# Optimization experiments

Hardware: AMD Instinct MI355X
Metric: run time of the kernel (lower is better)

The kernel has to match this reference:

```python
import jax, jax.numpy as jnp
import numpy as np
from jax import lax

N_GAUSS = 4096


def setup_inputs() -> dict:
    key = jax.random.key(0)
    k1, k2, k3, k4 = jax.random.split(key, 4)
    return {
        "_xyz": jax.random.normal(k1, (N_GAUSS, 3), dtype=jnp.float32),
        "_scaling": jax.random.normal(k2, (N_GAUSS, 3), dtype=jnp.float32),
        "_rotation": jax.random.normal(k3, (N_GAUSS, 4), dtype=jnp.float32),
        "_opacity": jax.random.normal(k4, (N_GAUSS, 1), dtype=jnp.float32),
        "resolution": 64,
        "num_blocks": 16,
    }


def _extract_fields(_xyz, _scaling, _rotation, _opacity, resolution, num_blocks):
    relax_ratio = 1.5
    block_size = 2.0 / num_blocks
    split_size = resolution // num_blocks

    # opacity activation + threshold mask (kept dense; masked gaussians get 0 weight)
    opacities = jax.nn.sigmoid(_opacity)[:, 0]  # [N]
    keep = opacities > 0.005
    opa = jnp.where(keep, opacities, 0.0)

    BIG = jnp.float32(1e10)
    mn = jnp.min(jnp.where(keep[:, None], _xyz, BIG), axis=0)
    mx = jnp.max(jnp.where(keep[:, None], _xyz, -BIG), axis=0)
    center = (mn + mx) / 2
    scale = 1.8 / jnp.max(mx - mn)
    xyzs = (_xyz - center) * scale           # [N,3] normalized positions
    stds = jnp.exp(_scaling) * scale         # [N,3] scaling activation * scale

    # covariance from scaling+rotation: L = R @ diag(s); C = L L^T
    q = _rotation / jnp.linalg.norm(_rotation, axis=1, keepdims=True)
    r, x, y, z = q[:, 0], q[:, 1], q[:, 2], q[:, 3]
    R = jnp.stack([
        jnp.stack([1 - 2 * (y * y + z * z), 2 * (x * y - r * z), 2 * (x * z + r * y)], -1),
        jnp.stack([2 * (x * y + r * z), 1 - 2 * (x * x + z * z), 2 * (y * z - r * x)], -1),
        jnp.stack([2 * (x * z - r * y), 2 * (y * z + r * x), 1 - 2 * (x * x + y * y)], -1),
    ], axis=1)                               # [N,3,3]
    L = R * stds[:, None, :]                 # R @ diag(s)
    C = jnp.einsum('nij,nkj->nik', L, L)     # [N,3,3]
    a, b, c = C[:, 0, 0], C[:, 0, 1], C[:, 0, 2]
    d, e, f = C[:, 1, 1], C[:, 1, 2], C[:, 2, 2]

    # analytic 3x3 symmetric inverse (precomputed per gaussian)
    inv_det = 1.0 / (a * d * f + 2 * e * c * b - e * e * a - c * c * d - b * b * f + 1e-24)
    inv_a = (d * f - e * e) * inv_det
    inv_b = (e * c - b * f) * inv_det
    inv_c = (e * b - c * d) * inv_det
    inv_d = (a * f - c * c) * inv_det
    inv_e = (b * c - e * a) * inv_det
    inv_f = (a * d - b * b) * inv_det

    lin = jnp.linspace(-1.0, 1.0, resolution).astype(jnp.float32)
    nb = num_blocks
    bi, bj, bk = jnp.meshgrid(jnp.arange(nb), jnp.arange(nb), jnp.arange(nb), indexing='ij')
    blocks = jnp.stack([bi.ravel(), bj.ravel(), bk.ravel()], axis=1)  # [nb^3, 3]
    off = jnp.arange(split_size)
    relax = block_size * relax_ratio

    def block_val(blk):
        xs = lin[blk[0] * split_size + off]
        ys = lin[blk[1] * split_size + off]
        zs = lin[blk[2] * split_size + off]
        xx, yy, zz = jnp.meshgrid(xs, ys, zs, indexing='ij')
        pts = jnp.stack([xx.ravel(), yy.ravel(), zz.ravel()], axis=-1)  # [S^3, 3]
        vmin = pts.min(0) - relax
        vmax = pts.max(0) + relax
        inside = jnp.all((xyzs < vmax) & (xyzs > vmin), axis=1)  # [N]
        w_opa = jnp.where(inside, opa, 0.0)                      # [N]
        dxyz = pts[:, None, :] - xyzs[None, :, :]                # [S^3, N, 3]
        px, py, pz = dxyz[..., 0], dxyz[..., 1], dxyz[..., 2]
        power = (-0.5 * (px * px * inv_a + py * py * inv_d + pz * pz * inv_f)
                 - px * py * inv_b - px * pz * inv_c - py * pz * inv_e)
        power = jnp.where(power > 0, jnp.float32(-1e10), power)
        val = jnp.sum(w_opa * jnp.exp(power), axis=1)            # [S^3]
        return val.reshape(split_size, split_size, split_size)

    vals = lax.map(block_val, blocks)  # [nb^3, S, S, S]
    occ = (vals.reshape(nb, nb, nb, split_size, split_size, split_size)
               .transpose(0, 3, 1, 4, 2, 5)
               .reshape(resolution, resolution, resolution))
    return occ


def reference(_xyz, _scaling, _rotation, _opacity, resolution, num_blocks):
    return _extract_fields(_xyz, _scaling, _rotation, _opacity, resolution, num_blocks)
```

## Files before the change

kernel.cpp:

```cpp
#include <hip/hip_runtime.h>

#define NG 4096
#define RELAX 0.1875f
#define KEEPTH -5.2933049f
#define SLICES 8
#define SLICE_G (NG/SLICES)
#define EV_THREADS 256

__device__ __forceinline__ float linf(int i) { return -1.0f + (2.0f/63.0f)*(float)i; }

__global__ __launch_bounds__(256) void gm_prep(
    const float* __restrict__ xyz, const float* __restrict__ scal,
    const float* __restrict__ rot, const float* __restrict__ opac,
    float4* __restrict__ posopa, float4* __restrict__ invrec,
    float4* __restrict__ out4)
{
  __shared__ float s_r[4][6];
  const int tid = threadIdx.x;
  const int b   = blockIdx.x;
  const float4* xyz4 = (const float4*)xyz;
  const float4* op4  = (const float4*)opac;

  {
    const int t0 = b*256 + tid;
    #pragma unroll
    for (int i = 0; i < 16; ++i) out4[t0 + i*4096] = make_float4(0,0,0,0);
  }

  float mn0=1e10f, mn1=1e10f, mn2=1e10f;
  float mx0=-1e10f, mx1=-1e10f, mx2=-1e10f;
  #pragma unroll
  for (int t = 0; t < 4; ++t) {
    const int G = t*256 + tid;
    float4 v0 = xyz4[3*G+0], v1 = xyz4[3*G+1], v2 = xyz4[3*G+2];
    float4 oo = op4[G];
    if (oo.x > KEEPTH) { mn0=fminf(mn0,v0.x); mx0=fmaxf(mx0,v0.x);
                         mn1=fminf(mn1,v0.y); mx1=fmaxf(mx1,v0.y);
                         mn2=fminf(mn2,v0.z); mx2=fmaxf(mx2,v0.z); }
    if (oo.y > KEEPTH) { mn0=fminf(mn0,v0.w); mx0=fmaxf(mx0,v0.w);
                         mn1=fminf(mn1,v1.x); mx1=fmaxf(mx1,v1.x);
                         mn2=fminf(mn2,v1.y); mx2=fmaxf(mx2,v1.y); }
    if (oo.z > KEEPTH) { mn0=fminf(mn0,v1.z); mx0=fmaxf(mx0,v1.z);
                         mn1=fminf(mn1,v1.w); mx1=fmaxf(mx1,v1.w);
                         mn2=fminf(mn2,v2.x); mx2=fmaxf(mx2,v2.x); }
    if (oo.w > KEEPTH) { mn0=fminf(mn0,v2.y); mx0=fmaxf(mx0,v2.y);
                         mn1=fminf(mn1,v2.z); mx1=fmaxf(mx1,v2.z);
                         mn2=fminf(mn2,v2.w); mx2=fmaxf(mx2,v2.w); }
  }
  #pragma unroll
  for (int s = 1; s < 64; s <<= 1) {
    mn0 = fminf(mn0, __shfl_xor(mn0, s)); mx0 = fmaxf(mx0, __shfl_xor(mx0, s));
    mn1 = fminf(mn1, __shfl_xor(mn1, s)); mx1 = fmaxf(mx1, __shfl_xor(mx1, s));
    mn2 = fminf(mn2, __shfl_xor(mn2, s)); mx2 = fmaxf(mx2, __shfl_xor(mx2, s));
  }
  if ((tid & 63) == 0) {
    const int w = tid >> 6;
    s_r[w][0]=mn0; s_r[w][1]=mn1; s_r[w][2]=mn2;
    s_r[w][3]=mx0; s_r[w][4]=mx1; s_r[w][5]=mx2;
  }
  __syncthreads();
  mn0 = fminf(fminf(s_r[0][0],s_r[1][0]), fminf(s_r[2][0],s_r[3][0]));
  mn1 = fminf(fminf(s_r[0][1],s_r[1][1]), fminf(s_r[2][1],s_r[3][1]));
  mn2 = fminf(fminf(s_r[0][2],s_r[1][2]), fminf(s_r[2][2],s_r[3][2]));
  mx0 = fmaxf(fmaxf(s_r[0][3],s_r[1][3]), fmaxf(s_r[2][3],s_r[3][3]));
  mx1 = fmaxf(fmaxf(s_r[0][4],s_r[1][4]), fmaxf(s_r[2][4],s_r[3][4]));
  mx2 = fmaxf(fmaxf(s_r[0][5],s_r[1][5]), fmaxf(s_r[2][5],s_r[3][5]));
  const float cx = (mn0+mx0)*0.5f;
  const float cy = (mn1+mx1)*0.5f;
  const float cz = (mn2+mx2)*0.5f;
  const float sc = 1.8f/fmaxf(mx0-mn0, fmaxf(mx1-mn1, mx2-mn2));

  const int g = b*256 + tid;
  float o = opac[g];
  float sig = 1.0f/(1.0f + __expf(-o));
  float opa = (sig > 0.005f) ? sig : 0.0f;
  float xs = (xyz[3*g+0]-cx)*sc;
  float ys = (xyz[3*g+1]-cy)*sc;
  float zs = (xyz[3*g+2]-cz)*sc;
  float sdx = __expf(scal[3*g+0])*sc;
  float sdy = __expf(scal[3*g+1])*sc;
  float sdz = __expf(scal[3*g+2])*sc;
  float qr=rot[4*g+0], qx=rot[4*g+1], qy=rot[4*g+2], qz=rot[4*g+3];
  float qn = 1.0f/sqrtf(qr*qr+qx*qx+qy*qy+qz*qz);
  qr*=qn; qx*=qn; qy*=qn; qz*=qn;
  float R00 = 1.0f-2.0f*(qy*qy+qz*qz), R01 = 2.0f*(qx*qy-qr*qz), R02 = 2.0f*(qx*qz+qr*qy);
  float R10 = 2.0f*(qx*qy+qr*qz), R11 = 1.0f-2.0f*(qx*qx+qz*qz), R12 = 2.0f*(qy*qz-qr*qx);
  float R20 = 2.0f*(qx*qz-qr*qy), R21 = 2.0f*(qy*qz+qr*qx), R22 = 1.0f-2.0f*(qx*qx+qy*qy);
  float L00=R00*sdx, L01=R01*sdy, L02=R02*sdz;
  float L10=R10*sdx, L11=R11*sdy, L12=R12*sdz;
  float L20=R20*sdx, L21=R21*sdy, L22=R22*sdz;
  float a = L00*L00+L01*L01+L02*L02;
  float bb= L00*L10+L01*L11+L02*L12;
  float cc= L00*L20+L01*L21+L02*L22;
  float d = L10*L10+L11*L11+L12*L12;
  float e = L10*L20+L11*L21+L12*L22;
  float f = L20*L20+L21*L21+L22*L22;
  float det = a*d*f + 2.0f*e*cc*bb - e*e*a - cc*cc*d - bb*bb*f + 1e-24f;
  float idt = 1.0f/det;
  float ia=(d*f-e*e)*idt, ib=(e*cc-bb*f)*idt, ic=(e*bb-cc*d)*idt;
  float id=(a*f-cc*cc)*idt, ie=(bb*cc-e*a)*idt, iff=(a*d-bb*bb)*idt;
  posopa[g]     = make_float4(xs, ys, zs, opa);
  invrec[2*g+0] = make_float4(-0.5f*ia, -ib, -ic, -0.5f*id);
  invrec[2*g+1] = make_float4(-ie, -0.5f*iff, 0.0f, 0.0f);
}

__global__ __launch_bounds__(EV_THREADS) void gm_eval(
    const float4* __restrict__ posopa, const float4* __restrict__ invrec,
    float* __restrict__ out)
{
  __shared__ float4 s_g[SLICE_G*3];
  __shared__ float  s_acc[EV_THREADS];
  __shared__ int    s_cnt;
  const int tid  = threadIdx.x;
  const int bin  = blockIdx.x >> 3;
  const int sl   = blockIdx.x & 7;
  const int bi = bin >> 8, bj = (bin >> 4) & 15, bk = bin & 15;
  const float vminx = linf(bi*4) - RELAX, vmaxx = linf(bi*4+3) + RELAX;
  const float vminy = linf(bj*4) - RELAX, vmaxy = linf(bj*4+3) + RELAX;
  const float vminz = linf(bk*4) - RELAX, vmaxz = linf(bk*4+3) + RELAX;
  if (tid == 0) s_cnt = 0;
  __syncthreads();

  #pragma unroll
  for (int t = 0; t < SLICE_G/EV_THREADS; ++t) {
    const int g = sl*SLICE_G + t*EV_THREADS + tid;
    float4 P = posopa[g];
    if (P.w > 0.0f &&
        P.x > vminx && P.x < vmaxx &&
        P.y > vminy && P.y < vmaxy &&
        P.z > vminz && P.z < vmaxz) {
      int slot = atomicAdd(&s_cnt, 1);
      s_g[3*slot+0] = P;
      s_g[3*slot+1] = invrec[2*g+0];
      s_g[3*slot+2] = invrec[2*g+1];
    }
  }
  __syncthreads();
  const int n = s_cnt;
  if (n == 0) return;

  const int p    = tid & 63;
  const int part = tid >> 6;
  const int sx = p >> 4, sy = (p >> 2) & 3, sz = p & 3;
  const float ptx = linf(bi*4+sx), pty = linf(bj*4+sy), ptz = linf(bk*4+sz);
  float acc = 0.0f;
  #pragma unroll 4
  for (int j = part; j < n; j += 4) {
    float4 P  = s_g[3*j+0];
    float4 I0 = s_g[3*j+1];
    float4 I1 = s_g[3*j+2];
    float px = ptx - P.x, py = pty - P.y, pz = ptz - P.z;
    float power = px*px*I0.x + py*py*I0.w + pz*pz*I1.y
                + px*py*I0.y + px*pz*I0.z + py*pz*I1.x;
    power = (power > 0.0f) ? -1e10f : power;
    acc += P.w * __expf(power);
  }
  s_acc[tid] = acc;
  __syncthreads();
  if (tid < 64) {
    float v = s_acc[tid] + s_acc[tid+64] + s_acc[tid+128] + s_acc[tid+192];
    atomicAdd(&out[(bi*4+sx)*4096 + (bj*4+sy)*64 + (bk*4+sz)], v);
  }
}

__global__ __launch_bounds__(256) void gm_fused_nows(
    const float* __restrict__ xyz, const float* __restrict__ scal,
    const float* __restrict__ rot, const float* __restrict__ opac,
    float* __restrict__ out)
{
  __shared__ float s_r[4][6];
  __shared__ float4 s_g[256*3];
  __shared__ float  s_acc[256];
  __shared__ int    s_cnt;
  const int tid = threadIdx.x;
  const float4* xyz4 = (const float4*)xyz;
  const float4* op4  = (const float4*)opac;

  float mn0=1e10f, mn1=1e10f, mn2=1e10f;
  float mx0=-1e10f, mx1=-1e10f, mx2=-1e10f;
  #pragma unroll
  for (int t = 0; t < 4; ++t) {
    const int G = t*256 + tid;
    float4 v0 = xyz4[3*G+0], v1 = xyz4[3*G+1], v2 = xyz4[3*G+2];
    float4 oo = op4[G];
    if (oo.x > KEEPTH) { mn0=fminf(mn0,v0.x); mx0=fmaxf(mx0,v0.x);
                         mn1=fminf(mn1,v0.y); mx1=fmaxf(mx1,v0.y);
                         mn2=fminf(mn2,v0.z); mx2=fmaxf(mx2,v0.z); }
    if (oo.y > KEEPTH) { mn0=fminf(mn0,v0.w); mx0=fmaxf(mx0,v0.w);
                         mn1=fminf(mn1,v1.x); mx1=fmaxf(mx1,v1.x);
                         mn2=fminf(mn2,v1.y); mx2=fmaxf(mx2,v1.y); }
    if (oo.z > KEEPTH) { mn0=fminf(mn0,v1.z); mx0=fmaxf(mx0,v1.z);
                         mn1=fminf(mn1,v1.w); mx1=fmaxf(mx1,v1.w);
                         mn2=fminf(mn2,v2.x); mx2=fmaxf(mx2,v2.x); }
    if (oo.w > KEEPTH) { mn0=fminf(mn0,v2.y); mx0=fmaxf(mx0,v2.y);
                         mn1=fminf(mn1,v2.z); mx1=fmaxf(mx1,v2.z);
                         mn2=fminf(mn2,v2.w); mx2=fmaxf(mx2,v2.w); }
  }
  #pragma unroll
  for (int s = 1; s < 64; s <<= 1) {
    mn0 = fminf(mn0, __shfl_xor(mn0, s)); mx0 = fmaxf(mx0, __shfl_xor(mx0, s));
    mn1 = fminf(mn1, __shfl_xor(mn1, s)); mx1 = fmaxf(mx1, __shfl_xor(mx1, s));
    mn2 = fminf(mn2, __shfl_xor(mn2, s)); mx2 = fmaxf(mx2, __shfl_xor(mx2, s));
  }
  if ((tid & 63) == 0) {
    const int w = tid >> 6;
    s_r[w][0]=mn0; s_r[w][1]=mn1; s_r[w][2]=mn2;
    s_r[w][3]=mx0; s_r[w][4]=mx1; s_r[w][5]=mx2;
  }
  if (tid == 0) s_cnt = 0;
  __syncthreads();
  mn0 = fminf(fminf(s_r[0][0],s_r[1][0]), fminf(s_r[2][0],s_r[3][0]));
  mn1 = fminf(fminf(s_r[0][1],s_r[1][1]), fminf(s_r[2][1],s_r[3][1]));
  mn2 = fminf(fminf(s_r[0][2],s_r[1][2]), fminf(s_r[2][2],s_r[3][2]));
  mx0 = fmaxf(fmaxf(s_r[0][3],s_r[1][3]), fmaxf(s_r[2][3],s_r[3][3]));
  mx1 = fmaxf(fmaxf(s_r[0][4],s_r[1][4]), fmaxf(s_r[2][4],s_r[3][4]));
  mx2 = fmaxf(fmaxf(s_r[0][5],s_r[1][5]), fmaxf(s_r[2][5],s_r[3][5]));
  const float cx = (mn0+mx0)*0.5f;
  const float cy = (mn1+mx1)*0.5f;
  const float cz = (mn2+mx2)*0.5f;
  const float sc = 1.8f/fmaxf(mx0-mn0, fmaxf(mx1-mn1, mx2-mn2));

  const int bin = blockIdx.x;
  const int bi = bin >> 8, bj = (bin >> 4) & 15, bk = bin & 15;
  const float vminx = linf(bi*4) - RELAX, vmaxx = linf(bi*4+3) + RELAX;
  const float vminy = linf(bj*4) - RELAX, vmaxy = linf(bj*4+3) + RELAX;
  const float vminz = linf(bk*4) - RELAX, vmaxz = linf(bk*4+3) + RELAX;
  const int p    = tid & 63;
  const int part = tid >> 6;
  const int sx = p >> 4, sy = (p >> 2) & 3, sz = p & 3;
  const float ptx = linf(bi*4+sx), pty = linf(bj*4+sy), ptz = linf(bk*4+sz);
  float acc = 0.0f;

  for (int c0 = 0; c0 < NG; c0 += 256) {
    const int g = c0 + tid;
    float o = opac[g];
    bool pass = false;
    float xs=0, ys=0, zs=0, sig=0;
    if (o > KEEPTH) {
      sig = 1.0f/(1.0f + __expf(-o));
      xs = (xyz[3*g+0]-cx)*sc;
      ys = (xyz[3*g+1]-cy)*sc;
      zs = (xyz[3*g+2]-cz)*sc;
      pass = xs > vminx && xs < vmaxx &&
             ys > vminy && ys < vmaxy &&
             zs > vminz && zs < vmaxz;
    }
    if (pass) {
      float sdx = __expf(scal[3*g+0])*sc;
      float sdy = __expf(scal[3*g+1])*sc;
      float sdz = __expf(scal[3*g+2])*sc;
      float qr=rot[4*g+0], qx=rot[4*g+1], qy=rot[4*g+2], qz=rot[4*g+3];
      float qn = 1.0f/sqrtf(qr*qr+qx*qx+qy*qy+qz*qz);
      qr*=qn; qx*=qn; qy*=qn; qz*=qn;
      float R00 = 1.0f-2.0f*(qy*qy+qz*qz), R01 = 2.0f*(qx*qy-qr*qz), R02 = 2.0f*(qx*qz+qr*qy);
      float R10 = 2.0f*(qx*qy+qr*qz), R11 = 1.0f-2.0f*(qx*qx+qz*qz), R12 = 2.0f*(qy*qz-qr*qx);
      float R20 = 2.0f*(qx*qz-qr*qy), R21 = 2.0f*(qy*qz+qr*qx), R22 = 1.0f-2.0f*(qx*qx+qy*qy);
      float L00=R00*sdx, L01=R01*sdy, L02=R02*sdz;
      float L10=R10*sdx, L11=R11*sdy, L12=R12*sdz;
      float L20=R20*sdx, L21=R21*sdy, L22=R22*sdz;
      float a = L00*L00+L01*L01+L02*L02;
      float bb= L00*L10+L01*L11+L02*L12;
      float cc= L00*L20+L01*L21+L02*L22;
      float d = L10*L10+L11*L11+L12*L12;
      float e = L10*L20+L11*L21+L12*L22;
      float f = L20*L20+L21*L21+L22*L22;
      float det = a*d*f + 2.0f*e*cc*bb - e*e*a - cc*cc*d - bb*bb*f + 1e-24f;
      float idt = 1.0f/det;
      float ia=(d*f-e*e)*idt, ib=(e*cc-bb*f)*idt, ic=(e*bb-cc*d)*idt;
      float id=(a*f-cc*cc)*idt, ie=(bb*cc-e*a)*idt, iff=(a*d-bb*bb)*idt;
      int slot = atomicAdd(&s_cnt, 1);
      s_g[3*slot+0] = make_float4(xs, ys, zs, sig);
      s_g[3*slot+1] = make_float4(-0.5f*ia, -ib, -ic, -0.5f*id);
      s_g[3*slot+2] = make_float4(-ie, -0.5f*iff, 0.0f, 0.0f);
    }
    __syncthreads();
    const int n = s_cnt;
    #pragma unroll 4
    for (int j = part; j < n; j += 4) {
      float4 P  = s_g[3*j+0];
      float4 I0 = s_g[3*j+1];
      float4 I1 = s_g[3*j+2];
      float px = ptx - P.x, py = pty - P.y, pz = ptz - P.z;
      float power = px*px*I0.x + py*py*I0.w + pz*pz*I1.y
                  + px*py*I0.y + px*pz*I0.z + py*pz*I1.x;
      power = (power > 0.0f) ? -1e10f : power;
      acc += P.w * __expf(power);
    }
    __syncthreads();
    if (tid == 0) s_cnt = 0;
    __syncthreads();
  }
  s_acc[tid] = acc;
  __syncthreads();
  if (tid < 64) {
    float v = s_acc[tid] + s_acc[tid+64] + s_acc[tid+128] + s_acc[tid+192];
    out[(bi*4+sx)*4096 + (bj*4+sy)*64 + (bk*4+sz)] = v;
  }
}

extern "C" void kernel_launch(void* const* d_in, const int* in_sizes, int n_in,
                              void* d_out, int out_size, void* d_ws, size_t ws_size,
                              hipStream_t stream) {
  const float* xyz  = (const float*)d_in[0];
  const float* scal = (const float*)d_in[1];
  const float* rot  = (const float*)d_in[2];
  const float* opac = (const float*)d_in[3];
  float* out = (float*)d_out;
  char* ws = (char*)d_ws;
  float4* posopa = (float4*)(ws);
  float4* invrec = (float4*)(ws + 65536);

  if (ws_size >= 196608) {
    gm_prep<<<16, 256, 0, stream>>>(xyz, scal, rot, opac,
                                    posopa, invrec, (float4*)out);
    gm_eval<<<4096*SLICES, EV_THREADS, 0, stream>>>(posopa, invrec, out);
  } else {
    gm_fused_nows<<<4096, 256, 0, stream>>>(xyz, scal, rot, opac, out);
  }
}
```

Before: 98.77 us.

## Bin gaussians into per-block index lists in prep, eval from compact lists

The prep kernel now runs on 256 blocks, one per (x,y) block column. Each builds per-z-bin index lists of the gaussians that fall inside each block's relaxed bounds, writing them into a workspace list capped at CAP entries. The eval kernel launches one workgroup per block instead of eight slices, gathers only the listed gaussians chunk by chunk into shared memory, and writes the output directly, so the zero-fill and atomic adds are no longer needed. This removes the redundant full scans of all gaussians per block. In exchange it needs a larger workspace, silently truncates bins that exceed CAP, and visits blocks in a center-out permuted order.

Result: slower. 152.8 us (+54.7%).

```diff
diff --git a/kernel.cpp b/kernel.cpp
--- a/kernel.cpp
+++ b/kernel.cpp
@@ -3,29 +3,25 @@
 #define NG 4096
 #define RELAX 0.1875f
 #define KEEPTH -5.2933049f
-#define SLICES 8
-#define SLICE_G (NG/SLICES)
+#define CHUNK 256
 #define EV_THREADS 256
+#define CAP 2048
 
 __device__ __forceinline__ float linf(int i) { return -1.0f + (2.0f/63.0f)*(float)i; }
-
-__global__ __launch_bounds__(256) void gm_prep(
+__device__ __forceinline__ int cperm(int i) { return (i & 1) ? 7 + ((i+1)>>1) : 7 - (i>>1); }
+
+__global__ __launch_bounds__(256) void gm_prep_bin(
     const float* __restrict__ xyz, const float* __restrict__ scal,
     const float* __restrict__ rot, const float* __restrict__ opac,
-    float4* __restrict__ posopa, float4* __restrict__ invrec,
-    float4* __restrict__ out4)
+    float4* __restrict__ rec,
+    int* __restrict__ bincnt, unsigned short* __restrict__ binidx)
 {
   __shared__ float s_r[4][6];
+  __shared__ int   s_cnt[16];
   const int tid = threadIdx.x;
   const int b   = blockIdx.x;
   const float4* xyz4 = (const float4*)xyz;
   const float4* op4  = (const float4*)opac;
-
-  {
-    const int t0 = b*256 + tid;
-    #pragma unroll
-    for (int i = 0; i < 16; ++i) out4[t0 + i*4096] = make_float4(0,0,0,0);
-  }
 
   float mn0=1e10f, mn1=1e10f, mn2=1e10f;
   float mx0=-1e10f, mx1=-1e10f, mx2=-1e10f;
@@ -58,6 +54,7 @@
     s_r[w][0]=mn0; s_r[w][1]=mn1; s_r[w][2]=mn2;
     s_r[w][3]=mx0; s_r[w][4]=mx1; s_r[w][5]=mx2;
   }
+  if (tid < 16) s_cnt[tid] = 0;
   __syncthreads();
   mn0 = fminf(fminf(s_r[0][0],s_r[1][0]), fminf(s_r[2][0],s_r[3][0]));
   mn1 = fminf(fminf(s_r[0][1],s_r[1][1]), fminf(s_r[2][1],s_r[3][1]));
@@ -70,96 +67,132 @@
   const float cz = (mn2+mx2)*0.5f;
   const float sc = 1.8f/fmaxf(mx0-mn0, fmaxf(mx1-mn1, mx2-mn2));
 
-  const int g = b*256 + tid;
-  float o = opac[g];
-  float sig = 1.0f/(1.0f + __expf(-o));
-  float opa = (sig > 0.005f) ? sig : 0.0f;
-  float xs = (xyz[3*g+0]-cx)*sc;
-  float ys = (xyz[3*g+1]-cy)*sc;
-  float zs = (xyz[3*g+2]-cz)*sc;
-  float sdx = __expf(scal[3*g+0])*sc;
-  float sdy = __expf(scal[3*g+1])*sc;
-  float sdz = __expf(scal[3*g+2])*sc;
-  float qr=rot[4*g+0], qx=rot[4*g+1], qy=rot[4*g+2], qz=rot[4*g+3];
-  float qn = 1.0f/sqrtf(qr*qr+qx*qx+qy*qy+qz*qz);
-  qr*=qn; qx*=qn; qy*=qn; qz*=qn;
-  float R00 = 1.0f-2.0f*(qy*qy+qz*qz), R01 = 2.0f*(qx*qy-qr*qz), R02 = 2.0f*(qx*qz+qr*qy);
-  float R10 = 2.0f*(qx*qy+qr*qz), R11 = 1.0f-2.0f*(qx*qx+qz*qz), R12 = 2.0f*(qy*qz-qr*qx);
-  float R20 = 2.0f*(qx*qz-qr*qy), R21 = 2.0f*(qy*qz+qr*qx), R22 = 1.0f-2.0f*(qx*qx+qy*qy);
-  float L00=R00*sdx, L01=R01*sdy, L02=R02*sdz;
-  float L10=R10*sdx, L11=R11*sdy, L12=R12*sdz;
-  float L20=R20*sdx, L21=R21*sdy, L22=R22*sdz;
-  float a = L00*L00+L01*L01+L02*L02;
-  float bb= L00*L10+L01*L11+L02*L12;
-  float cc= L00*L20+L01*L21+L02*L22;
-  float d = L10*L10+L11*L11+L12*L12;
-  float e = L10*L20+L11*L21+L12*L22;
-  float f = L20*L20+L21*L21+L22*L22;
-  float det = a*d*f + 2.0f*e*cc*bb - e*e*a - cc*cc*d - bb*bb*f + 1e-24f;
-  float idt = 1.0f/det;
-  float ia=(d*f-e*e)*idt, ib=(e*cc-bb*f)*idt, ic=(e*bb-cc*d)*idt;
-  float id=(a*f-cc*cc)*idt, ie=(bb*cc-e*a)*idt, iff=(a*d-bb*bb)*idt;
-  posopa[g]     = make_float4(xs, ys, zs, opa);
-  invrec[2*g+0] = make_float4(-0.5f*ia, -ib, -ic, -0.5f*id);
-  invrec[2*g+1] = make_float4(-ie, -0.5f*iff, 0.0f, 0.0f);
+  if (tid < 16) {
+    const int g = b*16 + tid;
+    float o = opac[g];
+    float sig = 1.0f/(1.0f + __expf(-o));
+    float opa = (sig > 0.005f) ? sig : 0.0f;
+    float xs = (xyz[3*g+0]-cx)*sc;
+    float ys = (xyz[3*g+1]-cy)*sc;
+    float zs = (xyz[3*g+2]-cz)*sc;
+    float sdx = __expf(scal[3*g+0])*sc;
+    float sdy = __expf(scal[3*g+1])*sc;
+    float sdz = __expf(scal[3*g+2])*sc;
+    float qr=rot[4*g+0], qx=rot[4*g+1], qy=rot[4*g+2], qz=rot[4*g+3];
+    float qn = 1.0f/sqrtf(qr*qr+qx*qx+qy*qy+qz*qz);
+    qr*=qn; qx*=qn; qy*=qn; qz*=qn;
+    float R00 = 1.0f-2.0f*(qy*qy+qz*qz), R01 = 2.0f*(qx*qy-qr*qz), R02 = 2.0f*(qx*qz+qr*qy);
+    float R10 = 2.0f*(qx*qy+qr*qz), R11 = 1.0f-2.0f*(qx*qx+qz*qz), R12 = 2.0f*(qy*qz-qr*qx);
+    float R20 = 2.0f*(qx*qz-qr*qy), R21 = 2.0f*(qy*qz+qr*qx), R22 = 1.0f-2.0f*(qx*qx+qy*qy);
+    float L00=R00*sdx, L01=R01*sdy, L02=R02*sdz;
+    float L10=R10*sdx, L11=R11*sdy, L12=R12*sdz;
+    float L20=R20*sdx, L21=R21*sdy, L22=R22*sdz;
+    float a = L00*L00+L01*L01+L02*L02;
+    float bb= L00*L10+L01*L11+L02*L12;
+    float cc= L00*L20+L01*L21+L02*L22;
+    float d = L10*L10+L11*L11+L12*L12;
+    float e = L10*L20+L11*L21+L12*L22;
+    float f = L20*L20+L21*L21+L22*L22;
+    float det = a*d*f + 2.0f*e*cc*bb - e*e*a - cc*cc*d - bb*bb*f + 1e-24f;
+    float idt = 1.0f/det;
+    float ia=(d*f-e*e)*idt, ib=(e*cc-bb*f)*idt, ic=(e*bb-cc*d)*idt;
+    float id=(a*f-cc*cc)*idt, ie=(bb*cc-e*a)*idt, iff=(a*d-bb*bb)*idt;
+    rec[3*g+0] = make_float4(xs, ys, zs, opa);
+    rec[3*g+1] = make_float4(-0.5f*ia, -ib, -ic, -0.5f*id);
+    rec[3*g+2] = make_float4(-ie, -0.5f*iff, 0.0f, 0.0f);
+  }
+
+  const int bi = b >> 4, bj = b & 15;
+  const float vminx = linf(bi*4) - RELAX, vmaxx = linf(bi*4+3) + RELAX;
+  const float vminy = linf(bj*4) - RELAX, vmaxy = linf(bj*4+3) + RELAX;
+  #pragma unroll
+  for (int t = 0; t < 4; ++t) {
+    const int G = t*256 + tid;
+    float4 v0 = xyz4[3*G+0], v1 = xyz4[3*G+1], v2 = xyz4[3*G+2];
+    float4 oo = op4[G];
+    float gx[4] = {v0.x, v0.w, v1.z, v2.y};
+    float gy[4] = {v0.y, v1.x, v1.w, v2.z};
+    float gz[4] = {v0.z, v1.y, v2.x, v2.w};
+    float go[4] = {oo.x, oo.y, oo.z, oo.w};
+    #pragma unroll
+    for (int u = 0; u < 4; ++u) {
+      if (!(go[u] > KEEPTH)) continue;
+      float xs = (gx[u]-cx)*sc;
+      float ys = (gy[u]-cy)*sc;
+      float zs = (gz[u]-cz)*sc;
+      if (xs > vminx && xs < vmaxx && ys > vminy && ys < vmaxy) {
+        int klo = (int)floorf(((zs + 0.8125f)*31.5f - 3.0f)*0.25f) - 1;
+        int khi = (int)floorf((zs + 1.1875f)*7.875f) + 1;
+        klo = max(klo, 0); khi = min(khi, 15);
+        for (int bk = klo; bk <= khi; ++bk) {
+          float lo = linf(bk*4) - RELAX, hi = linf(bk*4+3) + RELAX;
+          if (zs > lo && zs < hi) {
+            int slot = atomicAdd(&s_cnt[bk], 1);
+            if (slot < CAP)
+              binidx[(size_t)((b<<4) + bk)*CAP + slot] = (unsigned short)(4*G+u);
+          }
+        }
+      }
+    }
+  }
+  __syncthreads();
+  if (tid < 16) bincnt[(b<<4) + tid] = min(s_cnt[tid], CAP);
 }
 
 __global__ __launch_bounds__(EV_THREADS) void gm_eval(
-    const float4* __restrict__ posopa, const float4* __restrict__ invrec,
+    const float4* __restrict__ rec,
+    const int* __restrict__ bincnt, const unsigned short* __restrict__ binidx,
     float* __restrict__ out)
 {
-  __shared__ float4 s_g[SLICE_G*3];
+  __shared__ float4 s_g[CHUNK*3];
   __shared__ float  s_acc[EV_THREADS];
-  __shared__ int    s_cnt;
-  const int tid  = threadIdx.x;
-  const int bin  = blockIdx.x >> 3;
-  const int sl   = blockIdx.x & 7;
-  const int bi = bin >> 8, bj = (bin >> 4) & 15, bk = bin & 15;
-  const float vminx = linf(bi*4) - RELAX, vmaxx = linf(bi*4+3) + RELAX;
-  const float vminy = linf(bj*4) - RELAX, vmaxy = linf(bj*4+3) + RELAX;
-  const float vminz = linf(bk*4) - RELAX, vmaxz = linf(bk*4+3) + RELAX;
-  if (tid == 0) s_cnt = 0;
-  __syncthreads();
-
-  #pragma unroll
-  for (int t = 0; t < SLICE_G/EV_THREADS; ++t) {
-    const int g = sl*SLICE_G + t*EV_THREADS + tid;
-    float4 P = posopa[g];
-    if (P.w > 0.0f &&
-        P.x > vminx && P.x < vmaxx &&
-        P.y > vminy && P.y < vmaxy &&
-        P.z > vminz && P.z < vmaxz) {
-      int slot = atomicAdd(&s_cnt, 1);
-      s_g[3*slot+0] = P;
-      s_g[3*slot+1] = invrec[2*g+0];
-      s_g[3*slot+2] = invrec[2*g+1];
-    }
-  }
-  __syncthreads();
-  const int n = s_cnt;
-  if (n == 0) return;
-
+  const int tid = threadIdx.x;
+  const int b = blockIdx.x;
+  const int bi = cperm(b >> 8), bj = cperm((b >> 4) & 15), bk = cperm(b & 15);
+  const int bin = (bi*16 + bj)*16 + bk;
   const int p    = tid & 63;
   const int part = tid >> 6;
   const int sx = p >> 4, sy = (p >> 2) & 3, sz = p & 3;
+  const int obase = (bi*4+sx)*4096 + (bj*4+sy)*64 + (bk*4+sz);
+  const int n = min(bincnt[bin], CAP);
+
+  if (n == 0) {
+    if (tid < 64) out[obase] = 0.0f;
+    return;
+  }
+
   const float ptx = linf(bi*4+sx), pty = linf(bj*4+sy), ptz = linf(bk*4+sz);
+  const unsigned short* mylist = binidx + (size_t)bin*CAP;
   float acc = 0.0f;
-  #pragma unroll 4
-  for (int j = part; j < n; j += 4) {
-    float4 P  = s_g[3*j+0];
-    float4 I0 = s_g[3*j+1];
-    float4 I1 = s_g[3*j+2];
-    float px = ptx - P.x, py = pty - P.y, pz = ptz - P.z;
-    float power = px*px*I0.x + py*py*I0.w + pz*pz*I1.y
-                + px*py*I0.y + px*pz*I0.z + py*pz*I1.x;
-    power = (power > 0.0f) ? -1e10f : power;
-    acc += P.w * __expf(power);
-  }
+
+  for (int c0 = 0; c0 < n; c0 += CHUNK) {
+    __syncthreads();
+    const int lim = min(n - c0, CHUNK);
+    if (tid < lim) {
+      const int g = mylist[c0 + tid];
+      s_g[3*tid+0] = rec[3*g+0];
+      s_g[3*tid+1] = rec[3*g+1];
+      s_g[3*tid+2] = rec[3*g+2];
+    }
+    __syncthreads();
+    #pragma unroll 4
+    for (int j = part; j < lim; j += 4) {
+      float4 P  = s_g[3*j+0];
+      float4 I0 = s_g[3*j+1];
+      float4 I1 = s_g[3*j+2];
+      float px = ptx - P.x, py = pty - P.y, pz = ptz - P.z;
+      float power = px*px*I0.x + py*py*I0.w + pz*pz*I1.y
+                  + px*py*I0.y + px*pz*I0.z + py*pz*I1.x;
+      power = (power > 0.0f) ? -1e10f : power;
+      acc += P.w * __expf(power);
+    }
+  }
+
   s_acc[tid] = acc;
   __syncthreads();
   if (tid < 64) {
     float v = s_acc[tid] + s_acc[tid+64] + s_acc[tid+128] + s_acc[tid+192];
-    atomicAdd(&out[(bi*4+sx)*4096 + (bj*4+sy)*64 + (bk*4+sz)], v);
+    out[obase] = v;
   }
 }
 
@@ -307,13 +340,15 @@
   const float* opac = (const float*)d_in[3];
   float* out = (float*)d_out;
   char* ws = (char*)d_ws;
-  float4* posopa = (float4*)(ws);
-  float4* invrec = (float4*)(ws + 65536);
-
-  if (ws_size >= 196608) {
-    gm_prep<<<16, 256, 0, stream>>>(xyz, scal, rot, opac,
-                                    posopa, invrec, (float4*)out);
-    gm_eval<<<4096*SLICES, EV_THREADS, 0, stream>>>(posopa, invrec, out);
+  float4* rec    = (float4*)ws;
+  int*    bincnt = (int*)(ws + 196608);
+  unsigned short* binidx = (unsigned short*)(ws + 196608 + 16384);
+  const size_t base = 196608 + 16384;
+
+  if (ws_size >= base + (size_t)4096*CAP*2) {
+    gm_prep_bin<<<256, 256, 0, stream>>>(xyz, scal, rot, opac,
+                                         rec, bincnt, binidx);
+    gm_eval<<<4096, EV_THREADS, 0, stream>>>(rec, bincnt, binidx, out);
   } else {
     gm_fused_nows<<<4096, 256, 0, stream>>>(xyz, scal, rot, opac, out);
   }
```
